# Optimization experiments

Measured on AMD Instinct MI355X. Metric: run time of the kernel, lower is better.

The kernel has to match this reference:

```python
import jax, jax.numpy as jnp
import numpy as np
from jax import lax

B, H, W, C = 32, 64, 64, 192
DIN = 2 * C  # expand=2
EPS = 1e-5


def setup_inputs() -> dict:
    key = jax.random.key(0)
    ks = jax.random.split(key, 12)
    s = 0.02
    return {
        "x": jax.random.normal(ks[0], (B, H, W, C), dtype=jnp.float32),
        "norm_w": jnp.ones((C,), jnp.float32),
        "norm_b": jnp.zeros((C,), jnp.float32),
        "sel_w1": jax.random.normal(ks[1], (16, 4), jnp.float32) * 0.5,
        "sel_b1": jnp.zeros((16,), jnp.float32),
        "sel_w2": jax.random.normal(ks[2], (4, 16), jnp.float32) * 0.5,
        "sel_b2": jnp.zeros((4,), jnp.float32),
        "fc1_w": jax.random.normal(ks[3], (DIN, C), jnp.float32) * s,
        "fc1_b": jnp.zeros((DIN,), jnp.float32),
        "conv_w": jax.random.normal(ks[4], (DIN, 1, 3), jnp.float32) * 0.3,
        "conv_b": jnp.zeros((DIN,), jnp.float32),
        "fc2_w": jax.random.normal(ks[5], (C, DIN), jnp.float32) * s,
        "fc2_b": jnp.zeros((C,), jnp.float32),
    }


def _scan_dir(x, d):
    # x: [B,H,W,C] -> [B,L,C]; dirs = ['h','v','d','a'] (v and d are identical)
    b, h, w, c = x.shape
    if d == 0:  # 'h'
        return x.reshape(b, h * w, c)
    if d in (1, 2):  # 'v' / 'd': transpose then flatten
        return x.transpose(0, 2, 1, 3).reshape(b, w * h, c)
    # 'a': flip W, transpose, flatten
    return jnp.flip(x, axis=2).transpose(0, 2, 1, 3).reshape(b, w * h, c)


def _seq_block(s, fc1_w, fc1_b, conv_w, conv_b, fc2_w, fc2_b):
    # s: [B,L,C]
    h = jnp.einsum('blc,dc->bld', s, fc1_w) + fc1_b  # [B,L,DIN]
    hc = h.transpose(0, 2, 1)  # [B,DIN,L]
    hc = lax.conv_general_dilated(
        hc, conv_w, window_strides=(1,), padding=[(1, 1)],
        dimension_numbers=('NCH', 'OIH', 'NCH'),
        feature_group_count=conv_w.shape[0])
    hc = hc + conv_b[None, :, None]
    h = jax.nn.gelu(hc.transpose(0, 2, 1), approximate=False)
    return jnp.einsum('bld,cd->blc', h, fc2_w) + fc2_b


def reference(x, norm_w, norm_b, sel_w1, sel_b1, sel_w2, sel_b2,
              fc1_w, fc1_b, conv_w, conv_b, fc2_w, fc2_b):
    b, h, w, c = x.shape
    # LayerNorm over channels
    mu = x.mean(-1, keepdims=True)
    var = ((x - mu) ** 2).mean(-1, keepdims=True)
    xn = (x - mu) / jnp.sqrt(var + EPS) * norm_w + norm_b

    # Gradient-based direction selector
    g = xn.mean(-1)[:, None]  # [B,1,H,W]
    gp = jnp.pad(g, ((0, 0), (0, 0), (1, 1), (1, 1)), mode='reflect')
    grad_h = jnp.abs(gp[:, :, :, 2:] - gp[:, :, :, :-2])  # [B,1,H+2,W]
    grad_v = jnp.abs(gp[:, :, 2:, :] - gp[:, :, :-2, :])  # [B,1,H,W+2]
    sh = grad_h.mean(axis=(2, 3))  # [B,1]
    sv = grad_v.mean(axis=(2, 3))
    scores = jnp.concatenate([sh, sv, (sh + sv) / 2, jnp.abs(sh - sv)], axis=1)
    hid = jax.nn.relu(scores @ sel_w1.T + sel_b1)
    logits = hid @ sel_w2.T + sel_b2  # [B,4]
    dir_idx = jnp.argmax(logits, axis=-1)  # topk=1 -> argmax of softmax

    # Compute all 4 direction branches batched, then per-sample select
    outs = []
    for d in range(4):
        seq = _scan_dir(xn, d)
        proc = _seq_block(seq, fc1_w, fc1_b, conv_w, conv_b, fc2_w, fc2_b)
        outs.append(proc.reshape(b, h, w, c))  # unscan = plain reshape (as in source)
    stacked = jnp.stack(outs)  # [4,B,H,W,C]
    sel = stacked[dir_idx, jnp.arange(b)]  # [B,H,W,C]
    return x + sel
```

## Files before the change

kernel.cpp:

```cpp
#include <hip/hip_runtime.h>
#include <hip/hip_bf16.h>
#include <math.h>


typedef __bf16 bf16x8 __attribute__((ext_vector_type(8)));
typedef float f32x4 __attribute__((ext_vector_type(4)));
typedef __hip_bfloat16 hb;

#define XN_OFF   0
#define G_OFF    50331648
#define W1S_OFF  50855936
#define W2S_OFF  51003392
#define DIR_OFF  51150848

__device__ __forceinline__ float fast_gelu(float v) {
  float u = v * (0.7978845608f + 0.0356774081f * v * v);
  float e = __expf(2.f * u);
  float r = __builtin_amdgcn_rcpf(1.f + e);
  return v - v * r;
}

__device__ __forceinline__ unsigned short bf16bits(float f) {
  hb h = __float2bfloat16(f);
  return *reinterpret_cast<unsigned short*>(&h);
}

__global__ __launch_bounds__(256) void ln_wshuf_kernel(
    const float* __restrict__ x, const float* __restrict__ nw,
    const float* __restrict__ nb, hb* __restrict__ xn, float* __restrict__ g,
    const float* __restrict__ fc1_w, const float* __restrict__ fc2_w,
    hb* __restrict__ w1s, hb* __restrict__ w2s) {
  int t = threadIdx.x;
  if (blockIdx.x >= 8192) {
    int idx = (blockIdx.x - 8192) * 256 + t;
    const float* w; hb* o; int K, KS, li;
    if (idx < 73728) { w = fc1_w; o = w1s; K = 192; KS = 6;  li = idx; }
    else             { w = fc2_w; o = w2s; K = 384; KS = 12; li = idx - 73728; }
    int j = li & 7, lane = (li >> 3) & 63, f = li >> 9;
    int ks = f % KS, nt = f / KS;
    int n = nt * 16 + (lane & 15);
    int k = ks * 32 + ((lane >> 4) << 3) + j;
    o[li] = __float2bfloat16(w[n * K + k]);
    return;
  }
  __shared__ float4 xt[768];
  __shared__ unsigned int ytu[1536];
  __shared__ float snw[192], snb[192];
  long pixbase = (long)blockIdx.x * 16;
  const float4* x4 = (const float4*)(x + pixbase * 192);
  #pragma unroll
  for (int i = 0; i < 3; i++) xt[t + i * 256] = x4[t + i * 256];
  if (t < 192) { snw[t] = nw[t]; snb[t] = nb[t]; }
  __syncthreads();

  int p = t >> 4, sub = t & 15;
  const float4* row = xt + p * 48 + sub * 3;
  float4 f0 = row[0], f1 = row[1], f2 = row[2];
  float v[12] = {f0.x, f0.y, f0.z, f0.w, f1.x, f1.y, f1.z, f1.w,
                 f2.x, f2.y, f2.z, f2.w};
  float s1 = 0.f, s2 = 0.f;
  #pragma unroll
  for (int i = 0; i < 12; i++) { s1 += v[i]; s2 += v[i] * v[i]; }
  #pragma unroll
  for (int off = 8; off; off >>= 1) {
    s1 += __shfl_xor(s1, off);
    s2 += __shfl_xor(s2, off);
  }
  float mu = s1 * (1.f / 192.f);
  float var = s2 * (1.f / 192.f) - mu * mu;
  float rstd = rsqrtf(var + 1e-5f);
  int c0 = sub * 12;
  float ys[12], gs = 0.f;
  #pragma unroll
  for (int i = 0; i < 12; i++) {
    ys[i] = (v[i] - mu) * rstd * snw[c0 + i] + snb[c0 + i];
    gs += ys[i];
  }
  #pragma unroll
  for (int off = 8; off; off >>= 1) gs += __shfl_xor(gs, off);
  if (sub == 0) g[pixbase + p] = gs * (1.f / 192.f);
  unsigned int* yo = ytu + p * 96 + sub * 6;
  #pragma unroll
  for (int i = 0; i < 6; i++)
    yo[i] = (unsigned int)bf16bits(ys[2 * i]) |
            ((unsigned int)bf16bits(ys[2 * i + 1]) << 16);
  __syncthreads();
  const float4* yt4 = (const float4*)ytu;
  float4* o4 = (float4*)(xn + pixbase * 192);
  o4[t] = yt4[t];
  if (t < 128) o4[t + 256] = yt4[t + 256];
}

__global__ __launch_bounds__(256) void sel_kernel(
    const float* __restrict__ g, const float* __restrict__ w1,
    const float* __restrict__ b1, const float* __restrict__ w2,
    const float* __restrict__ b2, int* __restrict__ dir) {
  __shared__ float gt[64][65];
  __shared__ float red[8];
  int b = blockIdx.x, t = threadIdx.x;
  const float* gb = g + (long)b * 4096;
  for (int i = t; i < 4096; i += 256) gt[i >> 6][i & 63] = gb[i];
  __syncthreads();
  float ah = 0.f, av = 0.f;
  for (int i = t; i < 3968; i += 256) {
    int r = i / 62, j = i - r * 62 + 1;
    float d = fabsf(gt[r][j + 1] - gt[r][j - 1]);
    if (r == 1 || r == 62) d *= 2.f;
    ah += d;
  }
  for (int i = t; i < 3968; i += 256) {
    int r = (i >> 6) + 1, c = i & 63;
    float d = fabsf(gt[r + 1][c] - gt[r - 1][c]);
    if (c == 1 || c == 62) d *= 2.f;
    av += d;
  }
  #pragma unroll
  for (int off = 32; off; off >>= 1) {
    ah += __shfl_xor(ah, off);
    av += __shfl_xor(av, off);
  }
  if ((t & 63) == 0) { red[(t >> 6) * 2] = ah; red[(t >> 6) * 2 + 1] = av; }
  __syncthreads();
  if (t == 0) {
    float sh = 0.f, sv = 0.f;
    for (int w = 0; w < 4; w++) { sh += red[w * 2]; sv += red[w * 2 + 1]; }
    sh *= (1.f / 4224.f);
    sv *= (1.f / 4224.f);
    float sc[4] = {sh, sv, 0.5f * (sh + sv), fabsf(sh - sv)};
    float hid[16];
    #pragma unroll
    for (int i = 0; i < 16; i++) {
      float a = b1[i];
      for (int k = 0; k < 4; k++) a += sc[k] * w1[i * 4 + k];
      hid[i] = fmaxf(a, 0.f);
    }
    float best = -1e30f; int bi = 0;
    for (int j = 0; j < 4; j++) {
      float a = b2[j];
      for (int i = 0; i < 16; i++) a += hid[i] * w2[j * 16 + i];
      if (a > best) { best = a; bi = j; }
    }
    dir[b] = bi;
  }
}

#define SH_STR 196
__global__ __launch_bounds__(256, 5) void fused_kernel(
    const hb* __restrict__ xn, const hb* __restrict__ w1s, const hb* __restrict__ w2s,
    const float* __restrict__ fc1_b, const float* __restrict__ fc2_b,
    const float* __restrict__ conv_w, const float* __restrict__ conv_b,
    const float* __restrict__ x, const int* __restrict__ dirp,
    float* __restrict__ out) {
  __shared__ hb sH[2][32 * SH_STR];
  __shared__ float4 cvt[384];

  int b = blockIdx.y, mt = blockIdx.x;
  int dir = dirp[b];
  int l0 = mt * 30;
  int t = threadIdx.x;

  for (int d = t; d < 384; d += 256)
    cvt[d] = make_float4(conv_w[d * 3], conv_w[d * 3 + 1], conv_w[d * 3 + 2], conv_b[d]);

  int wave = t >> 6, lane = t & 63;
  int m16 = lane & 15, q = lane >> 4;
  int tile2 = wave & 1, nth = wave >> 1;
  const hb* xnb = xn + (long)b * 4096 * 192;

  float b1r[6], b2r[6];
  #pragma unroll
  for (int i = 0; i < 6; i++) b1r[i] = fc1_b[(wave * 6 + i) * 16 + m16];
  #pragma unroll
  for (int i = 0; i < 6; i++) b2r[i] = fc2_b[(nth * 6 + i) * 16 + m16];

  bf16x8 af[2][6];
  #pragma unroll
  for (int tl = 0; tl < 2; tl++) {
    int hr = tl * 16 + m16;
    int l = l0 - 1 + hr;
    int lc = min(max(l, 0), 4095);
    int src;
    if (dir == 0)      src = lc;
    else if (dir == 3) src = ((lc & 63) << 6) + 63 - (lc >> 6);
    else               src = ((lc & 63) << 6) + (lc >> 6);
    const bf16x8* ap = (const bf16x8*)(xnb + (long)src * 192) + q;
    #pragma unroll
    for (int ks = 0; ks < 6; ks++) af[tl][ks] = ap[ks * 4];
  }
  __syncthreads();

  {
    int buf = wave >> 1;
    int ntbase = wave * 6;
    #pragma unroll
    for (int i = 0; i < 6; i++) {
      int nt = ntbase + i;
      const bf16x8* bp = (const bf16x8*)w1s + (long)(nt * 6) * 64 + lane;
      f32x4 c0 = {0.f, 0.f, 0.f, 0.f}, c1 = {0.f, 0.f, 0.f, 0.f};
      #pragma unroll
      for (int ks = 0; ks < 6; ks++) {
        bf16x8 bf = bp[ks * 64];
        c0 = __builtin_amdgcn_mfma_f32_16x16x32_bf16(af[0][ks], bf, c0, 0, 0, 0);
        c1 = __builtin_amdgcn_mfma_f32_16x16x32_bf16(af[1][ks], bf, c1, 0, 0, 0);
      }
      float bias = b1r[i];
      int ncol = (nt - buf * 12) * 16 + m16;
      hb* s = &sH[buf][0];
      #pragma unroll
      for (int r = 0; r < 4; r++) {
        s[(q * 4 + r) * SH_STR + ncol]      = __float2bfloat16(c0[r] + bias);
        s[(16 + q * 4 + r) * SH_STR + ncol] = __float2bfloat16(c1[r] + bias);
      }
    }
  }
  __syncthreads();

  int hr = tile2 * 16 + m16;
  int l_c = l0 - 1 + hr;
  bool hm_ok = (l_c >= 1);
  bool hp_ok = (l_c <= 4094);
  int rm = hr > 0 ? hr - 1 : 0;
  int rp = hr < 31 ? hr + 1 : 31;
  bf16x8 z8 = {};
  bf16x8 af2[12];
  #pragma unroll
  for (int ks = 0; ks < 12; ks++) {
    int bb = ks / 6, kl = ks - bb * 6;
    int col = kl * 32 + q * 8;
    const hb* base = &sH[bb][0];
    bf16x8 vm = *(const bf16x8*)(base + rm * SH_STR + col);
    bf16x8 vc = *(const bf16x8*)(base + hr * SH_STR + col);
    bf16x8 vp = *(const bf16x8*)(base + rp * SH_STR + col);
    if (!hm_ok) vm = z8;
    if (!hp_ok) vp = z8;
    int d0 = ks * 32 + q * 8;
    bf16x8 o;
    #pragma unroll
    for (int j = 0; j < 8; j++) {
      float4 cw = cvt[d0 + j];
      float s = fmaf((float)vm[j], cw.x,
                fmaf((float)vc[j], cw.y,
                fmaf((float)vp[j], cw.z, cw.w)));
      o[j] = (__bf16)fast_gelu(s);
    }
    af2[ks] = o;
  }

  f32x4 acc[6];
  #pragma unroll
  for (int i = 0; i < 6; i++) acc[i] = (f32x4){0.f, 0.f, 0.f, 0.f};
  #pragma unroll
  for (int i2 = 0; i2 < 6; i2++) {
    int nt2 = nth * 6 + i2;
    const bf16x8* bp = (const bf16x8*)w2s + (long)(nt2 * 12) * 64 + lane;
    #pragma unroll
    for (int ks = 0; ks < 12; ks++)
      acc[i2] = __builtin_amdgcn_mfma_f32_16x16x32_bf16(af2[ks], bp[ks * 64], acc[i2], 0, 0, 0);
  }

  #pragma unroll
  for (int i2 = 0; i2 < 6; i2++) {
    int c = (nth * 6 + i2) * 16 + m16;
    float bias = b2r[i2];
    #pragma unroll
    for (int r = 0; r < 4; r++) {
      int hr_r = tile2 * 16 + q * 4 + r;
      int l_r = l0 - 1 + hr_r;
      if (hr_r >= 1 && hr_r <= 30 && l_r <= 4095) {
        long idx = ((long)b * 4096 + l_r) * 192 + c;
        out[idx] = x[idx] + acc[i2][r] + bias;
      }
    }
  }
}

extern "C" void kernel_launch(void* const* d_in, const int* in_sizes, int n_in,
                              void* d_out, int out_size, void* d_ws, size_t ws_size,
                              hipStream_t stream) {
  const float* x      = (const float*)d_in[0];
  const float* norm_w = (const float*)d_in[1];
  const float* norm_b = (const float*)d_in[2];
  const float* sel_w1 = (const float*)d_in[3];
  const float* sel_b1 = (const float*)d_in[4];
  const float* sel_w2 = (const float*)d_in[5];
  const float* sel_b2 = (const float*)d_in[6];
  const float* fc1_w  = (const float*)d_in[7];
  const float* fc1_b  = (const float*)d_in[8];
  const float* conv_w = (const float*)d_in[9];
  const float* conv_b = (const float*)d_in[10];
  const float* fc2_w  = (const float*)d_in[11];
  const float* fc2_b  = (const float*)d_in[12];
  float* out = (float*)d_out;
  char* ws = (char*)d_ws;

  hb* xn    = (hb*)(ws + XN_OFF);
  float* g  = (float*)(ws + G_OFF);
  hb* w1s   = (hb*)(ws + W1S_OFF);
  hb* w2s   = (hb*)(ws + W2S_OFF);
  int* dir  = (int*)(ws + DIR_OFF);

  ln_wshuf_kernel<<<8768, 256, 0, stream>>>(x, norm_w, norm_b, xn, g,
                                            fc1_w, fc2_w, w1s, w2s);
  sel_kernel<<<32, 256, 0, stream>>>(g, sel_w1, sel_b1, sel_w2, sel_b2, dir);
  dim3 gg(137, 32);
  fused_kernel<<<gg, 256, 0, stream>>>(xn, w1s, w2s, fc1_b, fc2_b,
                                       conv_w, conv_b, x, dir, out);
}
```

Measured before the change: 406.1 us.

## Recompute LayerNorm in fused kernel from per-pixel mean/rstd instead of storing bf16 xn

The first kernel no longer writes the normalized bf16 activation tensor. It stores only per-pixel mean and rstd, and the fused kernel reads fp32 x directly and applies the normalization while building the MFMA A fragments. This removes a large intermediate write and read, but each fused block now loads fp32 x, which is twice the bytes of the old bf16 xn, for its gathered rows. Biases move into LDS, and the occupancy hint drops from 5 to 4 blocks per SM, which may lower latency hiding.

```diff
diff --git a/kernel.cpp b/kernel.cpp
--- a/kernel.cpp
+++ b/kernel.cpp
@@ -7,11 +7,11 @@
 typedef float f32x4 __attribute__((ext_vector_type(4)));
 typedef __hip_bfloat16 hb;
 
-#define XN_OFF   0
-#define G_OFF    50331648
-#define W1S_OFF  50855936
-#define W2S_OFF  51003392
-#define DIR_OFF  51150848
+#define G_OFF    0
+#define MUR_OFF  524288
+#define W1S_OFF  1572864
+#define W2S_OFF  1720320
+#define DIR_OFF  1867776
 
 __device__ __forceinline__ float fast_gelu(float v) {
   float u = v * (0.7978845608f + 0.0356774081f * v * v);
@@ -20,14 +20,9 @@
   return v - v * r;
 }
 
-__device__ __forceinline__ unsigned short bf16bits(float f) {
-  hb h = __float2bfloat16(f);
-  return *reinterpret_cast<unsigned short*>(&h);
-}
-
-__global__ __launch_bounds__(256) void ln_wshuf_kernel(
+__global__ __launch_bounds__(256) void g_wshuf_kernel(
     const float* __restrict__ x, const float* __restrict__ nw,
-    const float* __restrict__ nb, hb* __restrict__ xn, float* __restrict__ g,
+    const float* __restrict__ nb, float* __restrict__ g, float2* __restrict__ mur,
     const float* __restrict__ fc1_w, const float* __restrict__ fc2_w,
     hb* __restrict__ w1s, hb* __restrict__ w2s) {
   int t = threadIdx.x;
@@ -44,7 +39,6 @@
     return;
   }
   __shared__ float4 xt[768];
-  __shared__ unsigned int ytu[1536];
   __shared__ float snw[192], snb[192];
   long pixbase = (long)blockIdx.x * 16;
   const float4* x4 = (const float4*)(x + pixbase * 192);
@@ -78,17 +72,10 @@
   }
   #pragma unroll
   for (int off = 8; off; off >>= 1) gs += __shfl_xor(gs, off);
-  if (sub == 0) g[pixbase + p] = gs * (1.f / 192.f);
-  unsigned int* yo = ytu + p * 96 + sub * 6;
-  #pragma unroll
-  for (int i = 0; i < 6; i++)
-    yo[i] = (unsigned int)bf16bits(ys[2 * i]) |
-            ((unsigned int)bf16bits(ys[2 * i + 1]) << 16);
-  __syncthreads();
-  const float4* yt4 = (const float4*)ytu;
-  float4* o4 = (float4*)(xn + pixbase * 192);
-  o4[t] = yt4[t];
-  if (t < 128) o4[t + 256] = yt4[t + 256];
+  if (sub == 0) {
+    g[pixbase + p] = gs * (1.f / 192.f);
+    mur[pixbase + p] = make_float2(mu, rstd);
+  }
 }
 
 __global__ __launch_bounds__(256) void sel_kernel(
@@ -145,33 +132,35 @@
 }
 
 #define SH_STR 196
-__global__ __launch_bounds__(256, 5) void fused_kernel(
-    const hb* __restrict__ xn, const hb* __restrict__ w1s, const hb* __restrict__ w2s,
+__global__ __launch_bounds__(256, 4) void fused_kernel(
+    const float* __restrict__ x, const float* __restrict__ nw,
+    const float* __restrict__ nb, const float2* __restrict__ mur,
+    const hb* __restrict__ w1s, const hb* __restrict__ w2s,
     const float* __restrict__ fc1_b, const float* __restrict__ fc2_b,
     const float* __restrict__ conv_w, const float* __restrict__ conv_b,
-    const float* __restrict__ x, const int* __restrict__ dirp,
-    float* __restrict__ out) {
+    const int* __restrict__ dirp, float* __restrict__ out) {
   __shared__ hb sH[2][32 * SH_STR];
   __shared__ float4 cvt[384];
+  __shared__ float2 snwb[192];
+  __shared__ float sB1[384];
+  __shared__ float sB2[192];
 
   int b = blockIdx.y, mt = blockIdx.x;
   int dir = dirp[b];
   int l0 = mt * 30;
   int t = threadIdx.x;
 
-  for (int d = t; d < 384; d += 256)
+  for (int d = t; d < 384; d += 256) {
     cvt[d] = make_float4(conv_w[d * 3], conv_w[d * 3 + 1], conv_w[d * 3 + 2], conv_b[d]);
+    sB1[d] = fc1_b[d];
+  }
+  if (t < 192) { sB2[t] = fc2_b[t]; snwb[t] = make_float2(nw[t], nb[t]); }
 
   int wave = t >> 6, lane = t & 63;
   int m16 = lane & 15, q = lane >> 4;
-  int tile2 = wave & 1, nth = wave >> 1;
-  const hb* xnb = xn + (long)b * 4096 * 192;
-
-  float b1r[6], b2r[6];
-  #pragma unroll
-  for (int i = 0; i < 6; i++) b1r[i] = fc1_b[(wave * 6 + i) * 16 + m16];
-  #pragma unroll
-  for (int i = 0; i < 6; i++) b2r[i] = fc2_b[(nth * 6 + i) * 16 + m16];
+  const float* xb = x + (long)b * 4096 * 192;
+  const float2* murb = mur + (long)b * 4096;
+  __syncthreads();
 
   bf16x8 af[2][6];
   #pragma unroll
@@ -183,11 +172,30 @@
     if (dir == 0)      src = lc;
     else if (dir == 3) src = ((lc & 63) << 6) + 63 - (lc >> 6);
     else               src = ((lc & 63) << 6) + (lc >> 6);
-    const bf16x8* ap = (const bf16x8*)(xnb + (long)src * 192) + q;
-    #pragma unroll
-    for (int ks = 0; ks < 6; ks++) af[tl][ks] = ap[ks * 4];
-  }
-  __syncthreads();
+    const float4* xp = (const float4*)(xb + (long)src * 192);
+    float2 mr = murb[src];
+    float mu = mr.x, rstd = mr.y;
+    #pragma unroll
+    for (int ks = 0; ks < 6; ks++) {
+      float4 u0 = xp[ks * 8 + q * 2];
+      float4 u1 = xp[ks * 8 + q * 2 + 1];
+      int cc = ks * 32 + q * 8;
+      bf16x8 o;
+      #pragma unroll
+      for (int j = 0; j < 4; j++) {
+        float2 wb = snwb[cc + j];
+        float xv = (&u0.x)[j];
+        o[j] = (__bf16)((xv - mu) * rstd * wb.x + wb.y);
+      }
+      #pragma unroll
+      for (int j = 0; j < 4; j++) {
+        float2 wb = snwb[cc + 4 + j];
+        float xv = (&u1.x)[j];
+        o[4 + j] = (__bf16)((xv - mu) * rstd * wb.x + wb.y);
+      }
+      af[tl][ks] = o;
+    }
+  }
 
   {
     int buf = wave >> 1;
@@ -203,7 +211,7 @@
         c0 = __builtin_amdgcn_mfma_f32_16x16x32_bf16(af[0][ks], bf, c0, 0, 0, 0);
         c1 = __builtin_amdgcn_mfma_f32_16x16x32_bf16(af[1][ks], bf, c1, 0, 0, 0);
       }
-      float bias = b1r[i];
+      float bias = sB1[nt * 16 + m16];
       int ncol = (nt - buf * 12) * 16 + m16;
       hb* s = &sH[buf][0];
       #pragma unroll
@@ -215,6 +223,7 @@
   }
   __syncthreads();
 
+  int tile2 = wave & 1, nth = wave >> 1;
   int hr = tile2 * 16 + m16;
   int l_c = l0 - 1 + hr;
   bool hm_ok = (l_c >= 1);
@@ -261,7 +270,7 @@
   #pragma unroll
   for (int i2 = 0; i2 < 6; i2++) {
     int c = (nth * 6 + i2) * 16 + m16;
-    float bias = b2r[i2];
+    float bias = sB2[c];
     #pragma unroll
     for (int r = 0; r < 4; r++) {
       int hr_r = tile2 * 16 + q * 4 + r;
@@ -293,16 +302,16 @@
   float* out = (float*)d_out;
   char* ws = (char*)d_ws;
 
-  hb* xn    = (hb*)(ws + XN_OFF);
-  float* g  = (float*)(ws + G_OFF);
-  hb* w1s   = (hb*)(ws + W1S_OFF);
-  hb* w2s   = (hb*)(ws + W2S_OFF);
-  int* dir  = (int*)(ws + DIR_OFF);
-
-  ln_wshuf_kernel<<<8768, 256, 0, stream>>>(x, norm_w, norm_b, xn, g,
-                                            fc1_w, fc2_w, w1s, w2s);
+  float* g    = (float*)(ws + G_OFF);
+  float2* mur = (float2*)(ws + MUR_OFF);
+  hb* w1s     = (hb*)(ws + W1S_OFF);
+  hb* w2s     = (hb*)(ws + W2S_OFF);
+  int* dir    = (int*)(ws + DIR_OFF);
+
+  g_wshuf_kernel<<<8768, 256, 0, stream>>>(x, norm_w, norm_b, g, mur,
+                                           fc1_w, fc2_w, w1s, w2s);
   sel_kernel<<<32, 256, 0, stream>>>(g, sel_w1, sel_b1, sel_w2, sel_b2, dir);
   dim3 gg(137, 32);
-  fused_kernel<<<gg, 256, 0, stream>>>(xn, w1s, w2s, fc1_b, fc2_b,
-                                       conv_w, conv_b, x, dir, out);
-}
+  fused_kernel<<<gg, 256, 0, stream>>>(x, norm_w, norm_b, mur, w1s, w2s,
+                                       fc1_b, fc2_b, conv_w, conv_b, dir, out);
+}
```

Result: faster. 394.8 us (-2.8%).

## Split conv+GELU work across waves and exchange halves via shared memory

Applied to the files above, without the earlier changes.

Each wave previously computed the depthwise conv and GELU for all 12 K-slices of its rows, so waves sharing the same rows repeated that work twice. Now each wave computes only its half (6 slices) and writes it to shared memory; the other half is read back from the partner wave's results. The fc1 and fc2 biases are staged in shared memory instead of held in registers, and the occupancy hint drops from 5 to 4 blocks. This halves the conv/GELU arithmetic but adds two block-wide barriers and an LDS round trip, and the occupancy hint may lower the number of resident blocks.

```diff
diff --git a/kernel.cpp b/kernel.cpp
--- a/kernel.cpp
+++ b/kernel.cpp
@@ -145,7 +145,7 @@
 }
 
 #define SH_STR 196
-__global__ __launch_bounds__(256, 5) void fused_kernel(
+__global__ __launch_bounds__(256, 4) void fused_kernel(
     const hb* __restrict__ xn, const hb* __restrict__ w1s, const hb* __restrict__ w2s,
     const float* __restrict__ fc1_b, const float* __restrict__ fc2_b,
     const float* __restrict__ conv_w, const float* __restrict__ conv_b,
@@ -153,25 +153,23 @@
     float* __restrict__ out) {
   __shared__ hb sH[2][32 * SH_STR];
   __shared__ float4 cvt[384];
+  __shared__ float sB1[384];
+  __shared__ float sB2[192];
 
   int b = blockIdx.y, mt = blockIdx.x;
   int dir = dirp[b];
   int l0 = mt * 30;
   int t = threadIdx.x;
 
-  for (int d = t; d < 384; d += 256)
+  for (int d = t; d < 384; d += 256) {
     cvt[d] = make_float4(conv_w[d * 3], conv_w[d * 3 + 1], conv_w[d * 3 + 2], conv_b[d]);
+    sB1[d] = fc1_b[d];
+  }
+  if (t < 192) sB2[t] = fc2_b[t];
 
   int wave = t >> 6, lane = t & 63;
   int m16 = lane & 15, q = lane >> 4;
-  int tile2 = wave & 1, nth = wave >> 1;
   const hb* xnb = xn + (long)b * 4096 * 192;
-
-  float b1r[6], b2r[6];
-  #pragma unroll
-  for (int i = 0; i < 6; i++) b1r[i] = fc1_b[(wave * 6 + i) * 16 + m16];
-  #pragma unroll
-  for (int i = 0; i < 6; i++) b2r[i] = fc2_b[(nth * 6 + i) * 16 + m16];
 
   bf16x8 af[2][6];
   #pragma unroll
@@ -203,7 +201,7 @@
         c0 = __builtin_amdgcn_mfma_f32_16x16x32_bf16(af[0][ks], bf, c0, 0, 0, 0);
         c1 = __builtin_amdgcn_mfma_f32_16x16x32_bf16(af[1][ks], bf, c1, 0, 0, 0);
       }
-      float bias = b1r[i];
+      float bias = sB1[nt * 16 + m16];
       int ncol = (nt - buf * 12) * 16 + m16;
       hb* s = &sH[buf][0];
       #pragma unroll
@@ -215,6 +213,7 @@
   }
   __syncthreads();
 
+  int tile2 = wave & 1, nth = wave >> 1;
   int hr = tile2 * 16 + m16;
   int l_c = l0 - 1 + hr;
   bool hm_ok = (l_c >= 1);
@@ -222,18 +221,17 @@
   int rm = hr > 0 ? hr - 1 : 0;
   int rp = hr < 31 ? hr + 1 : 31;
   bf16x8 z8 = {};
-  bf16x8 af2[12];
-  #pragma unroll
-  for (int ks = 0; ks < 12; ks++) {
-    int bb = ks / 6, kl = ks - bb * 6;
-    int col = kl * 32 + q * 8;
-    const hb* base = &sH[bb][0];
+  const hb* base = &sH[nth][0];
+  bf16x8 cg[6];
+  #pragma unroll
+  for (int i = 0; i < 6; i++) {
+    int col = i * 32 + q * 8;
     bf16x8 vm = *(const bf16x8*)(base + rm * SH_STR + col);
     bf16x8 vc = *(const bf16x8*)(base + hr * SH_STR + col);
     bf16x8 vp = *(const bf16x8*)(base + rp * SH_STR + col);
     if (!hm_ok) vm = z8;
     if (!hp_ok) vp = z8;
-    int d0 = ks * 32 + q * 8;
+    int d0 = (nth * 6 + i) * 32 + q * 8;
     bf16x8 o;
     #pragma unroll
     for (int j = 0; j < 8; j++) {
@@ -243,7 +241,24 @@
                 fmaf((float)vp[j], cw.z, cw.w)));
       o[j] = (__bf16)fast_gelu(s);
     }
-    af2[ks] = o;
+    cg[i] = o;
+  }
+  __syncthreads();
+
+  {
+    hb* wb = &sH[nth][0];
+    #pragma unroll
+    for (int i = 0; i < 6; i++)
+      *(bf16x8*)(wb + hr * SH_STR + i * 32 + q * 8) = cg[i];
+  }
+  __syncthreads();
+
+  bf16x8 og[6];
+  {
+    const hb* ob = &sH[nth ^ 1][0];
+    #pragma unroll
+    for (int i = 0; i < 6; i++)
+      og[i] = *(const bf16x8*)(ob + hr * SH_STR + i * 32 + q * 8);
   }
 
   f32x4 acc[6];
@@ -254,14 +269,19 @@
     int nt2 = nth * 6 + i2;
     const bf16x8* bp = (const bf16x8*)w2s + (long)(nt2 * 12) * 64 + lane;
     #pragma unroll
-    for (int ks = 0; ks < 12; ks++)
-      acc[i2] = __builtin_amdgcn_mfma_f32_16x16x32_bf16(af2[ks], bp[ks * 64], acc[i2], 0, 0, 0);
+    for (int i = 0; i < 6; i++)
+      acc[i2] = __builtin_amdgcn_mfma_f32_16x16x32_bf16(
+          cg[i], bp[(nth * 6 + i) * 64], acc[i2], 0, 0, 0);
+    #pragma unroll
+    for (int i = 0; i < 6; i++)
+      acc[i2] = __builtin_amdgcn_mfma_f32_16x16x32_bf16(
+          og[i], bp[((nth ^ 1) * 6 + i) * 64], acc[i2], 0, 0, 0);
   }
 
   #pragma unroll
   for (int i2 = 0; i2 < 6; i2++) {
     int c = (nth * 6 + i2) * 16 + m16;
-    float bias = b2r[i2];
+    float bias = sB2[c];
     #pragma unroll
     for (int r = 0; r < 4; r++) {
       int hr_r = tile2 * 16 + q * 4 + r;
```

New measurement: 340.5 us. 16.2% less time.
